# Kernel optimization log

Hardware: AMD Instinct MI355X
Metric: run time of the kernel (lower is better)

The kernel has to match this reference:

```python
import jax, jax.numpy as jnp
import numpy as np

NUM_USER = 200000
NUM_ITEM = 100000
DIM = 64
NUM_LAYER = 2  # hardcoded in LightGCN.__init__ (lgn_single(..., num_layer=2))
AVG_DEG = 16
N = NUM_USER + NUM_ITEM
E = N * AVG_DEG
BATCH = 16384


def setup_inputs() -> dict:
    key = jax.random.key(0)
    k = jax.random.split(key, 8)
    emb_user = jax.random.normal(k[0], (NUM_USER, DIM), jnp.float32) * 0.05
    emb_item = jax.random.normal(k[1], (NUM_ITEM, DIM), jnp.float32) * 0.05
    # COO sparse normalized adjacency: out[row] += vals * x[col]
    graph_row = jax.random.randint(k[2], (E,), 0, N, dtype=jnp.int32)
    graph_col = jax.random.randint(k[3], (E,), 0, N, dtype=jnp.int32)
    graph_vals = jax.random.uniform(k[4], (E,), jnp.float32) / AVG_DEG
    user_nodes = jax.random.randint(k[5], (BATCH,), 0, NUM_USER, dtype=jnp.int32)
    pos_item_nodes = jax.random.randint(k[6], (BATCH,), 0, NUM_ITEM, dtype=jnp.int32) + NUM_USER
    neg_item_nodes = jax.random.randint(k[7], (BATCH,), 0, NUM_ITEM, dtype=jnp.int32) + NUM_USER
    return {
        "emb_user": emb_user,
        "emb_item": emb_item,
        "graph_vals": graph_vals,
        "graph_row": graph_row,
        "graph_col": graph_col,
        "user_nodes": user_nodes,
        "pos_item_nodes": pos_item_nodes,
        "neg_item_nodes": neg_item_nodes,
    }


def _spmm(vals, row, col, x):
    # torch.sparse.mm(graph, x) with graph in COO form
    return jax.ops.segment_sum(vals[:, None] * x[col], row, num_segments=N)


def reference(emb_user, emb_item, graph_vals, graph_row, graph_col,
              user_nodes, pos_item_nodes, neg_item_nodes):
    # LGN_single.forward: concat, propagate, mean over layer stack
    all_emb = jnp.concatenate([emb_user, emb_item], axis=0)  # [N, D]
    acc = all_emb
    e = all_emb
    for _ in range(NUM_LAYER):
        e = _spmm(graph_vals, graph_row, graph_col, e)
        acc = acc + e
    light_out = acc / (NUM_LAYER + 1)  # mean of stacked embeddings
    # LightGCN.forward: gather + elementwise dot scores
    u = light_out[user_nodes]          # [B, D]
    p = light_out[pos_item_nodes]      # [B, D]
    n = light_out[neg_item_nodes]      # [B, D]
    pos_scores = jnp.sum(u * p, axis=1)
    neg_scores = jnp.sum(u * n, axis=1)
    return jnp.stack([pos_scores, neg_scores])  # [2, B]
```

## Files before the change

kernel.cpp:

```cpp
#include <hip/hip_runtime.h>

#define DIM 64
#define CHUNK 16384
#define MAXNB 512
#define BSHIFT 10
#define RPB 1024
#define PADMASK 7

union H8 { uint4 u; _Float16 h[8]; };
union H4 { uint2 u; _Float16 h[4]; };

__device__ __forceinline__ int blockScan256(int v, int* sh) {
    int t = threadIdx.x;
    sh[t] = v;
    __syncthreads();
    for (int off = 1; off < 256; off <<= 1) {
        int x = (t >= off) ? sh[t - off] : 0;
        __syncthreads();
        sh[t] += x;
        __syncthreads();
    }
    return sh[t];
}


__global__ void conv2_k(const float* __restrict__ u, const float* __restrict__ it,
                        int nu, int ntot, unsigned short* __restrict__ o) {
    int i = blockIdx.x * blockDim.x + threadIdx.x;
    int stride = gridDim.x * blockDim.x;
    int n8 = ntot >> 3;
    for (int t = i; t < n8; t += stride) {
        int e = t * 8;
        const float* src = (e < nu) ? (u + e) : (it + (e - nu));
        float4 x = *(const float4*)src;
        float4 y = *(const float4*)(src + 4);
        H8 v;
        v.h[0] = (_Float16)x.x; v.h[1] = (_Float16)x.y;
        v.h[2] = (_Float16)x.z; v.h[3] = (_Float16)x.w;
        v.h[4] = (_Float16)y.x; v.h[5] = (_Float16)y.y;
        v.h[6] = (_Float16)y.z; v.h[7] = (_Float16)y.w;
        ((uint4*)o)[t] = v.u;
    }
}


__global__ void p1a_hist(const int* __restrict__ row, int E, int NB,
                         int* __restrict__ counts) {
    __shared__ int h[MAXNB];
    for (int b = threadIdx.x; b < NB; b += 256) h[b] = 0;
    __syncthreads();
    int base = blockIdx.x * CHUNK;
    int end = min(base + CHUNK, E);
    int vend = base + ((end - base) & ~3);
    for (int i = base + threadIdx.x * 4; i < vend; i += 1024) {
        int4 r = *(const int4*)(row + i);
        atomicAdd(&h[r.x >> BSHIFT], 1);
        atomicAdd(&h[r.y >> BSHIFT], 1);
        atomicAdd(&h[r.z >> BSHIFT], 1);
        atomicAdd(&h[r.w >> BSHIFT], 1);
    }
    for (int i = vend + threadIdx.x; i < end; i += 256) atomicAdd(&h[row[i] >> BSHIFT], 1);
    __syncthreads();
    int blk = blockIdx.x;
    for (int b = threadIdx.x; b < NB; b += 256) counts[(size_t)blk * NB + b] = h[b];
}

__global__ void p1b_scan(int* __restrict__ counts, int NBLK, int NB,
                         int* __restrict__ bucketTotal) {
    int b = blockIdx.x, t = threadIdx.x;
    __shared__ int sh[256];
    int v[8];
    int run = 0;
#pragma unroll
    for (int i = 0; i < 8; i++) {
        int idx = t * 8 + i;
        int c = (idx < NBLK) ? counts[(size_t)idx * NB + b] : 0;
        v[i] = run;
        run += c;
    }
    int inc = blockScan256(run, sh);
    int excl = inc - run;
#pragma unroll
    for (int i = 0; i < 8; i++) {
        int idx = t * 8 + i;
        if (idx < NBLK) counts[(size_t)idx * NB + b] = v[i] + excl;
    }
    if (t == 255) bucketTotal[b] = sh[255];
}

__global__ void p_scan_tot(const int* __restrict__ bucketTotal, int NB,
                           int* __restrict__ bucketStart) {
    int t = threadIdx.x;
    __shared__ int sh[256];
    int v[8];
    int run = 0;
#pragma unroll
    for (int i = 0; i < 8; i++) {
        int idx = t * 8 + i;
        int c = (idx < NB) ? bucketTotal[idx] : 0;
        v[i] = run;
        run += c;
    }
    int inc = blockScan256(run, sh);
    int excl = inc - run;
#pragma unroll
    for (int i = 0; i < 8; i++) {
        int idx = t * 8 + i;
        if (idx < NB) bucketStart[idx] = v[i] + excl;
    }
    if (t == 255) bucketStart[NB] = sh[255];
}

__global__ void p1c_scatter(const int* __restrict__ row, const int* __restrict__ col,
                            const float* __restrict__ vals, int E, int NB,
                            const int* __restrict__ counts, const int* __restrict__ bucketStart,
                            int2* __restrict__ bdata) {
    __shared__ int cur[MAXNB];
    int blk = blockIdx.x;
    for (int b = threadIdx.x; b < NB; b += 256)
        cur[b] = bucketStart[b] + counts[(size_t)blk * NB + b];
    __syncthreads();
    int base = blk * CHUNK;
    int end = min(base + CHUNK, E);
    int vend = base + ((end - base) & ~3);
    for (int i = base + threadIdx.x * 4; i < vend; i += 1024) {
        int4 r = *(const int4*)(row + i);
        int4 c = *(const int4*)(col + i);
        float4 v = *(const float4*)(vals + i);
        int p0 = atomicAdd(&cur[r.x >> BSHIFT], 1);
        int p1 = atomicAdd(&cur[r.y >> BSHIFT], 1);
        int p2 = atomicAdd(&cur[r.z >> BSHIFT], 1);
        int p3 = atomicAdd(&cur[r.w >> BSHIFT], 1);
        bdata[p0] = make_int2(((r.x & (RPB - 1)) << 20) | c.x, __float_as_int(v.x));
        bdata[p1] = make_int2(((r.y & (RPB - 1)) << 20) | c.y, __float_as_int(v.y));
        bdata[p2] = make_int2(((r.z & (RPB - 1)) << 20) | c.z, __float_as_int(v.z));
        bdata[p3] = make_int2(((r.w & (RPB - 1)) << 20) | c.w, __float_as_int(v.w));
    }
    for (int i = vend + threadIdx.x; i < end; i += 256) {
        int r = row[i];
        int p = atomicAdd(&cur[r >> BSHIFT], 1);
        bdata[p] = make_int2(((r & (RPB - 1)) << 20) | col[i], __float_as_int(vals[i]));
    }
}

__global__ void p2_group(const int2* __restrict__ bdata, const int* __restrict__ bucketStart,
                         int NB, int N, int padSlop,
                         int* __restrict__ rowStart, int* __restrict__ rowLen,
                         int2* __restrict__ pairs) {
    __shared__ int hist[RPB];
    __shared__ int sh[256];
    __shared__ int cur[RPB];
    int b = blockIdx.x, t = threadIdx.x;
    int s0 = bucketStart[b], s1 = bucketStart[b + 1];
    int pbase = s0 + b * padSlop;
    for (int i = t; i < RPB; i += 256) hist[i] = 0;
    __syncthreads();
    for (int i = s0 + t; i < s1; i += 256)
        atomicAdd(&hist[(bdata[i].x >> 20) & (RPB - 1)], 1);
    __syncthreads();
    int v[4];
    int run = 0;
#pragma unroll
    for (int i = 0; i < 4; i++) {
        int h = hist[t * 4 + i];
        int hp = (h + PADMASK) & ~PADMASK;
        v[i] = run;
        run += hp;
    }
    int inc = blockScan256(run, sh);
    int excl = inc - run;
#pragma unroll
    for (int i = 0; i < 4; i++) {
        int r = (b << BSHIFT) + t * 4 + i;
        int st = excl + v[i];
        if (r < N) {
            int h = hist[t * 4 + i];
            rowStart[r] = pbase + st;
            rowLen[r] = (h + PADMASK) & ~PADMASK;
        }
        cur[t * 4 + i] = st;
    }
    __syncthreads();
    for (int i = s0 + t; i < s1; i += 256) {
        int2 e = bdata[i];
        int rl = (e.x >> 20) & (RPB - 1);
        int pos = atomicAdd(&cur[rl], 1);
        pairs[pbase + pos] = make_int2((e.x & 0xFFFFF) << 7, e.y);
    }
    __syncthreads();
#pragma unroll
    for (int i = 0; i < 4; i++) {
        int h = hist[t * 4 + i];
        int hp = (h + PADMASK) & ~PADMASK;
        int st = excl + v[i];
        for (int p = st + h; p < st + hp; p++)
            pairs[pbase + p] = make_int2(0, 0);
    }
}


__global__ void spmm1_k(const unsigned short* __restrict__ emb16,
                        const int* __restrict__ rowStart, const int* __restrict__ rowLen,
                        const int2* __restrict__ pairs,
                        int n_total, unsigned short* __restrict__ e1) {
    int wave = (blockIdx.x * blockDim.x + threadIdx.x) >> 6;
    int lane = threadIdx.x & 63;
    if (wave >= n_total) return;
    int eg = lane >> 3, dp = lane & 7;
    unsigned off0 = dp * 16u;
    const char* base = (const char*)emb16;
    int len = rowLen[wave];
    const int2* pp = pairs + rowStart[wave];
    float aA[8] = {0.f, 0.f, 0.f, 0.f, 0.f, 0.f, 0.f, 0.f};
    float aB[8] = {0.f, 0.f, 0.f, 0.f, 0.f, 0.f, 0.f, 0.f};
    int k = 0;
    for (; k + 16 <= len; k += 16) {
        int4 q = *(const int4*)(pp + k + 2 * eg);
        H8 g0, g1;
        g0.u = *(const uint4*)(base + ((unsigned)q.x + off0));
        g1.u = *(const uint4*)(base + ((unsigned)q.z + off0));
        float v0 = __int_as_float(q.y), v1 = __int_as_float(q.w);
#pragma unroll
        for (int i = 0; i < 8; i++) aA[i] += (float)g0.h[i] * v0;
#pragma unroll
        for (int i = 0; i < 8; i++) aB[i] += (float)g1.h[i] * v1;
    }
    if (k < len) {
        int2 p = pp[k + eg];
        H8 g0;
        g0.u = *(const uint4*)(base + ((unsigned)p.x + off0));
        float v0 = __int_as_float(p.y);
#pragma unroll
        for (int i = 0; i < 8; i++) aA[i] += (float)g0.h[i] * v0;
    }
    float s[8];
#pragma unroll
    for (int i = 0; i < 8; i++) s[i] = aA[i] + aB[i];
#pragma unroll
    for (int m = 8; m <= 32; m <<= 1) {
#pragma unroll
        for (int i = 0; i < 8; i++) s[i] += __shfl_xor(s[i], m);
    }
    if (eg == 0) {
        H8 o;
#pragma unroll
        for (int i = 0; i < 8; i++) o.h[i] = (_Float16)s[i];
        *(uint4*)(e1 + (size_t)wave * DIM + dp * 8) = o.u;
    }
}


__global__ void final_k(const float* __restrict__ emb_user, const float* __restrict__ emb_item,
                        int n_user, const unsigned short* __restrict__ e1,
                        const int* __restrict__ rowStart, const int* __restrict__ rowLen,
                        const int2* __restrict__ pairs,
                        const int* __restrict__ u_nodes, const int* __restrict__ p_nodes,
                        const int* __restrict__ n_nodes, int B, float* __restrict__ out) {
    int wave = (blockIdx.x * blockDim.x + threadIdx.x) >> 6;
    int lane = threadIdx.x & 63;
    if (wave >= B) return;
    int eg = lane >> 4, dp = lane & 15;
    unsigned off0 = dp * 8u;
    const char* base = (const char*)e1;
    int nid[3] = {u_nodes[wave], p_nodes[wave], n_nodes[wave]};
    float l[3][4];
#pragma unroll
    for (int j = 0; j < 3; j++) {
        int r = nid[j];
        const float* base0 = (r < n_user) ? (emb_user + (size_t)r * DIM)
                                          : (emb_item + (size_t)(r - n_user) * DIM);
        float4 l0 = *(const float4*)(base0 + dp * 4);
        H4 t1;
        t1.u = *(const uint2*)(e1 + (size_t)r * DIM + dp * 4);
        float acc[4];
        acc[0] = l0.x + (float)t1.h[0];
        acc[1] = l0.y + (float)t1.h[1];
        acc[2] = l0.z + (float)t1.h[2];
        acc[3] = l0.w + (float)t1.h[3];
        int len = rowLen[r];
        const int2* pp = pairs + rowStart[r];
        float a0[4] = {0.f, 0.f, 0.f, 0.f}, a1[4] = {0.f, 0.f, 0.f, 0.f};
        float a2[4] = {0.f, 0.f, 0.f, 0.f}, a3[4] = {0.f, 0.f, 0.f, 0.f};
        int k = 0;
        for (; k + 16 <= len; k += 16) {
            int4 q0 = *(const int4*)(pp + k + 2 * eg);
            int4 q1 = *(const int4*)(pp + k + 8 + 2 * eg);
            H4 g0, g1, g2, g3;
            g0.u = *(const uint2*)(base + ((unsigned)q0.x + off0));
            g1.u = *(const uint2*)(base + ((unsigned)q0.z + off0));
            g2.u = *(const uint2*)(base + ((unsigned)q1.x + off0));
            g3.u = *(const uint2*)(base + ((unsigned)q1.z + off0));
            float v0 = __int_as_float(q0.y), v1 = __int_as_float(q0.w);
            float v2 = __int_as_float(q1.y), v3 = __int_as_float(q1.w);
#pragma unroll
            for (int i = 0; i < 4; i++) {
                a0[i] += (float)g0.h[i] * v0;
                a1[i] += (float)g1.h[i] * v1;
                a2[i] += (float)g2.h[i] * v2;
                a3[i] += (float)g3.h[i] * v3;
            }
        }
        for (; k < len; k += 8) {
            int4 q0 = *(const int4*)(pp + k + 2 * eg);
            H4 g0, g1;
            g0.u = *(const uint2*)(base + ((unsigned)q0.x + off0));
            g1.u = *(const uint2*)(base + ((unsigned)q0.z + off0));
            float v0 = __int_as_float(q0.y), v1 = __int_as_float(q0.w);
#pragma unroll
            for (int i = 0; i < 4; i++) {
                a0[i] += (float)g0.h[i] * v0;
                a1[i] += (float)g1.h[i] * v1;
            }
        }
        float s[4];
#pragma unroll
        for (int i = 0; i < 4; i++) s[i] = (a0[i] + a1[i]) + (a2[i] + a3[i]);
#pragma unroll
        for (int i = 0; i < 4; i++) {
            s[i] += __shfl_xor(s[i], 16);
            s[i] += __shfl_xor(s[i], 32);
        }
#pragma unroll
        for (int i = 0; i < 4; i++) l[j][i] = (acc[i] + s[i]) * (1.0f / 3.0f);
    }
    float ps = l[0][0] * l[1][0] + l[0][1] * l[1][1] + l[0][2] * l[1][2] + l[0][3] * l[1][3];
    float ns = l[0][0] * l[2][0] + l[0][1] * l[2][1] + l[0][2] * l[2][2] + l[0][3] * l[2][3];
    ps += __shfl_xor(ps, 1); ns += __shfl_xor(ns, 1);
    ps += __shfl_xor(ps, 2); ns += __shfl_xor(ns, 2);
    ps += __shfl_xor(ps, 4); ns += __shfl_xor(ns, 4);
    ps += __shfl_xor(ps, 8); ns += __shfl_xor(ns, 8);
    if (lane == 0) {
        out[wave] = ps;
        out[B + wave] = ns;
    }
}

extern "C" void kernel_launch(void* const* d_in, const int* in_sizes, int n_in,
                              void* d_out, int out_size, void* d_ws, size_t ws_size,
                              hipStream_t stream) {
    const float* emb_user = (const float*)d_in[0];
    const float* emb_item = (const float*)d_in[1];
    const float* gvals    = (const float*)d_in[2];
    const int*   grow     = (const int*)d_in[3];
    const int*   gcol     = (const int*)d_in[4];
    const int*   unodes   = (const int*)d_in[5];
    const int*   pnodes   = (const int*)d_in[6];
    const int*   nnodes   = (const int*)d_in[7];
    float* out = (float*)d_out;

    int n_user = in_sizes[0] / DIM;
    int n_item = in_sizes[1] / DIM;
    int N = n_user + n_item;
    int E = in_sizes[2];
    int B = in_sizes[5];
    int NB = (N + RPB - 1) >> BSHIFT;
    int NBLK = (E + CHUNK - 1) / CHUNK;
    int padSlop = RPB * PADMASK;

    char* ws = (char*)d_ws;
    size_t off = 0;
    auto alloc = [&](size_t bytes) -> void* {
        void* p = ws + off;
        off = (off + bytes + 255) & ~(size_t)255;
        return p;
    };
    size_t embBytes = (size_t)N * DIM * 2;
    size_t countsBytes = (size_t)NBLK * NB * 4;
    size_t regionBBytes = (size_t)E * 8 > embBytes ? (size_t)E * 8 : embBytes;
    size_t regionABytes = countsBytes > embBytes ? countsBytes : embBytes;
    size_t pairsBytes = ((size_t)E + (size_t)NB * padSlop) * 8;

    int*  rowStart    = (int*)alloc((size_t)N * 4);
    int*  rowLen      = (int*)alloc((size_t)N * 4);
    int*  bucketTotal = (int*)alloc((size_t)MAXNB * 4);
    int*  bucketStart = (int*)alloc((size_t)(MAXNB + 1) * 4);
    int2* pairs       = (int2*)alloc(pairsBytes);
    char* regionB = (char*)alloc(regionBBytes);
    int2*           bdata = (int2*)regionB;
    unsigned short* emb16 = (unsigned short*)regionB;
    char* regionA = (char*)alloc(regionABytes);
    int*            counts = (int*)regionA;
    unsigned short* e1     = (unsigned short*)regionA;
    (void)n_in; (void)out_size; (void)ws_size;

    p1a_hist<<<NBLK, 256, 0, stream>>>(grow, E, NB, counts);
    p1b_scan<<<NB, 256, 0, stream>>>(counts, NBLK, NB, bucketTotal);
    p_scan_tot<<<1, 256, 0, stream>>>(bucketTotal, NB, bucketStart);
    p1c_scatter<<<NBLK, 256, 0, stream>>>(grow, gcol, gvals, E, NB, counts, bucketStart, bdata);
    p2_group<<<NB, 256, 0, stream>>>(bdata, bucketStart, NB, N, padSlop,
                                     rowStart, rowLen, pairs);

    conv2_k<<<2048, 256, 0, stream>>>(emb_user, emb_item, n_user * DIM, N * DIM, emb16);

    spmm1_k<<<(N + 3) / 4, 256, 0, stream>>>(emb16, rowStart, rowLen, pairs, N, e1);
    final_k<<<(B + 3) / 4, 256, 0, stream>>>(emb_user, emb_item, n_user, e1,
                                             rowStart, rowLen, pairs,
                                             unodes, pnodes, nnodes, B, out);
}
```

Before: 300.9 us.

## Stage bucket scatter in LDS and overlap fp16 conversion with histogram

The scatter kernel now sorts each chunk's edges by bucket in shared memory first. It then writes each bucket's run contiguously to global memory, replacing random per-edge global writes with coalesced ones. The per-block local offsets come from differencing the scanned counts. The fp16 embedding conversion is folded into extra blocks of the histogram kernel when the workspace allows separate buffers, removing a serial launch. CHUNK is halved so the 64KB staging buffer fits in LDS, which doubles the number of blocks and the size of the counts matrix.

```diff
diff --git a/kernel.cpp b/kernel.cpp
--- a/kernel.cpp
+++ b/kernel.cpp
@@ -1,11 +1,12 @@
 #include <hip/hip_runtime.h>
 
 #define DIM 64
-#define CHUNK 16384
+#define CHUNK 8192
 #define MAXNB 512
 #define BSHIFT 10
 #define RPB 1024
 #define PADMASK 7
+#define CONVB 768
 
 union H8 { uint4 u; _Float16 h[8]; };
 union H4 { uint2 u; _Float16 h[4]; };
@@ -23,13 +24,12 @@
     return sh[t];
 }
 
-
-__global__ void conv2_k(const float* __restrict__ u, const float* __restrict__ it,
-                        int nu, int ntot, unsigned short* __restrict__ o) {
-    int i = blockIdx.x * blockDim.x + threadIdx.x;
-    int stride = gridDim.x * blockDim.x;
+__device__ __forceinline__ void convBody(const float* __restrict__ u,
+                                         const float* __restrict__ it,
+                                         int nu, int ntot, unsigned short* __restrict__ o,
+                                         int start, int stride) {
     int n8 = ntot >> 3;
-    for (int t = i; t < n8; t += stride) {
+    for (int t = start; t < n8; t += stride) {
         int e = t * 8;
         const float* src = (e < nu) ? (u + e) : (it + (e - nu));
         float4 x = *(const float4*)src;
@@ -44,25 +44,38 @@
 }
 
 
-__global__ void p1a_hist(const int* __restrict__ row, int E, int NB,
-                         int* __restrict__ counts) {
+__global__ void p1a_conv(const int* __restrict__ row, int E, int NB,
+                         int* __restrict__ counts,
+                         const float* __restrict__ u, const float* __restrict__ it,
+                         int nu, int ntot, unsigned short* __restrict__ o, int NBLK) {
     __shared__ int h[MAXNB];
-    for (int b = threadIdx.x; b < NB; b += 256) h[b] = 0;
-    __syncthreads();
-    int base = blockIdx.x * CHUNK;
-    int end = min(base + CHUNK, E);
-    int vend = base + ((end - base) & ~3);
-    for (int i = base + threadIdx.x * 4; i < vend; i += 1024) {
-        int4 r = *(const int4*)(row + i);
-        atomicAdd(&h[r.x >> BSHIFT], 1);
-        atomicAdd(&h[r.y >> BSHIFT], 1);
-        atomicAdd(&h[r.z >> BSHIFT], 1);
-        atomicAdd(&h[r.w >> BSHIFT], 1);
-    }
-    for (int i = vend + threadIdx.x; i < end; i += 256) atomicAdd(&h[row[i] >> BSHIFT], 1);
-    __syncthreads();
     int blk = blockIdx.x;
-    for (int b = threadIdx.x; b < NB; b += 256) counts[(size_t)blk * NB + b] = h[b];
+    if (blk < NBLK) {
+        for (int b = threadIdx.x; b < NB; b += 256) h[b] = 0;
+        __syncthreads();
+        int base = blk * CHUNK;
+        int end = min(base + CHUNK, E);
+        int vend = base + ((end - base) & ~3);
+        for (int i = base + threadIdx.x * 4; i < vend; i += 1024) {
+            int4 r = *(const int4*)(row + i);
+            atomicAdd(&h[r.x >> BSHIFT], 1);
+            atomicAdd(&h[r.y >> BSHIFT], 1);
+            atomicAdd(&h[r.z >> BSHIFT], 1);
+            atomicAdd(&h[r.w >> BSHIFT], 1);
+        }
+        for (int i = vend + threadIdx.x; i < end; i += 256) atomicAdd(&h[row[i] >> BSHIFT], 1);
+        __syncthreads();
+        for (int b = threadIdx.x; b < NB; b += 256) counts[(size_t)blk * NB + b] = h[b];
+    } else {
+        int nConv = gridDim.x - NBLK;
+        convBody(u, it, nu, ntot, o, (blk - NBLK) * 256 + threadIdx.x, nConv * 256);
+    }
+}
+
+__global__ void conv2_k(const float* __restrict__ u, const float* __restrict__ it,
+                        int nu, int ntot, unsigned short* __restrict__ o) {
+    convBody(u, it, nu, ntot, o, blockIdx.x * blockDim.x + threadIdx.x,
+             gridDim.x * blockDim.x);
 }
 
 __global__ void p1b_scan(int* __restrict__ counts, int NBLK, int NB,
@@ -112,34 +125,66 @@
 }
 
 __global__ void p1c_scatter(const int* __restrict__ row, const int* __restrict__ col,
-                            const float* __restrict__ vals, int E, int NB,
-                            const int* __restrict__ counts, const int* __restrict__ bucketStart,
-                            int2* __restrict__ bdata) {
+                            const float* __restrict__ vals, int E, int NB, int NBLK,
+                            const int* __restrict__ counts, const int* __restrict__ bucketTotal,
+                            const int* __restrict__ bucketStart, int2* __restrict__ bdata) {
+    __shared__ int2 stage[CHUNK];
     __shared__ int cur[MAXNB];
-    int blk = blockIdx.x;
-    for (int b = threadIdx.x; b < NB; b += 256)
-        cur[b] = bucketStart[b] + counts[(size_t)blk * NB + b];
-    __syncthreads();
+    __shared__ int rawcnt[MAXNB];
+    __shared__ int sh[256];
+    int blk = blockIdx.x, t = threadIdx.x;
     int base = blk * CHUNK;
     int end = min(base + CHUNK, E);
+    int v[2];
+    int run = 0;
+#pragma unroll
+    for (int i = 0; i < 2; i++) {
+        int b = t * 2 + i;
+        int c = 0;
+        if (b < NB) {
+            int s0 = counts[(size_t)blk * NB + b];
+            int s1 = (blk + 1 < NBLK) ? counts[(size_t)(blk + 1) * NB + b] : bucketTotal[b];
+            c = s1 - s0;
+            rawcnt[b] = c;
+        }
+        v[i] = run;
+        run += c;
+    }
+    int inc = blockScan256(run, sh);
+    int excl = inc - run;
+#pragma unroll
+    for (int i = 0; i < 2; i++) {
+        int b = t * 2 + i;
+        if (b < NB) cur[b] = excl + v[i];
+    }
+    __syncthreads();
     int vend = base + ((end - base) & ~3);
-    for (int i = base + threadIdx.x * 4; i < vend; i += 1024) {
+    for (int i = base + t * 4; i < vend; i += 1024) {
         int4 r = *(const int4*)(row + i);
         int4 c = *(const int4*)(col + i);
-        float4 v = *(const float4*)(vals + i);
+        float4 w = *(const float4*)(vals + i);
         int p0 = atomicAdd(&cur[r.x >> BSHIFT], 1);
         int p1 = atomicAdd(&cur[r.y >> BSHIFT], 1);
         int p2 = atomicAdd(&cur[r.z >> BSHIFT], 1);
         int p3 = atomicAdd(&cur[r.w >> BSHIFT], 1);
-        bdata[p0] = make_int2(((r.x & (RPB - 1)) << 20) | c.x, __float_as_int(v.x));
-        bdata[p1] = make_int2(((r.y & (RPB - 1)) << 20) | c.y, __float_as_int(v.y));
-        bdata[p2] = make_int2(((r.z & (RPB - 1)) << 20) | c.z, __float_as_int(v.z));
-        bdata[p3] = make_int2(((r.w & (RPB - 1)) << 20) | c.w, __float_as_int(v.w));
-    }
-    for (int i = vend + threadIdx.x; i < end; i += 256) {
+        stage[p0] = make_int2(((r.x & (RPB - 1)) << 20) | c.x, __float_as_int(w.x));
+        stage[p1] = make_int2(((r.y & (RPB - 1)) << 20) | c.y, __float_as_int(w.y));
+        stage[p2] = make_int2(((r.z & (RPB - 1)) << 20) | c.z, __float_as_int(w.z));
+        stage[p3] = make_int2(((r.w & (RPB - 1)) << 20) | c.w, __float_as_int(w.w));
+    }
+    for (int i = vend + t; i < end; i += 256) {
         int r = row[i];
         int p = atomicAdd(&cur[r >> BSHIFT], 1);
-        bdata[p] = make_int2(((r & (RPB - 1)) << 20) | col[i], __float_as_int(vals[i]));
+        stage[p] = make_int2(((r & (RPB - 1)) << 20) | col[i], __float_as_int(vals[i]));
+    }
+    __syncthreads();
+    int wv = t >> 6, lane = t & 63;
+    for (int b = wv; b < NB; b += 4) {
+        int cnt = rawcnt[b];
+        int lo = cur[b] - cnt;
+        int gb = bucketStart[b] + counts[(size_t)blk * NB + b];
+        for (int i = lane; i < cnt; i += 64)
+            bdata[gb + i] = stage[lo + i];
     }
 }
 
@@ -357,6 +402,17 @@
     int NBLK = (E + CHUNK - 1) / CHUNK;
     int padSlop = RPB * PADMASK;
 
+    auto align256 = [](size_t x) { return (x + 255) & ~(size_t)255; };
+    size_t embBytes = (size_t)N * DIM * 2;
+    size_t countsBytes = (size_t)NBLK * NB * 4;
+    size_t bdataBytes = (size_t)E * 8;
+    size_t regionABytes = countsBytes > embBytes ? countsBytes : embBytes;
+    size_t pairsBytes = ((size_t)E + (size_t)NB * padSlop) * 8;
+    size_t fixedBytes = align256((size_t)N * 4) * 2 + align256((size_t)MAXNB * 4) +
+                        align256((size_t)(MAXNB + 1) * 4) + align256(pairsBytes) +
+                        align256(regionABytes);
+    bool sepEmb = fixedBytes + align256(bdataBytes) + align256(embBytes) <= ws_size;
+
     char* ws = (char*)d_ws;
     size_t off = 0;
     auto alloc = [&](size_t bytes) -> void* {
@@ -364,33 +420,38 @@
         off = (off + bytes + 255) & ~(size_t)255;
         return p;
     };
-    size_t embBytes = (size_t)N * DIM * 2;
-    size_t countsBytes = (size_t)NBLK * NB * 4;
-    size_t regionBBytes = (size_t)E * 8 > embBytes ? (size_t)E * 8 : embBytes;
-    size_t regionABytes = countsBytes > embBytes ? countsBytes : embBytes;
-    size_t pairsBytes = ((size_t)E + (size_t)NB * padSlop) * 8;
-
     int*  rowStart    = (int*)alloc((size_t)N * 4);
     int*  rowLen      = (int*)alloc((size_t)N * 4);
     int*  bucketTotal = (int*)alloc((size_t)MAXNB * 4);
     int*  bucketStart = (int*)alloc((size_t)(MAXNB + 1) * 4);
     int2* pairs       = (int2*)alloc(pairsBytes);
-    char* regionB = (char*)alloc(regionBBytes);
-    int2*           bdata = (int2*)regionB;
-    unsigned short* emb16 = (unsigned short*)regionB;
+    int2* bdata;
+    unsigned short* emb16;
+    if (sepEmb) {
+        bdata = (int2*)alloc(bdataBytes);
+        emb16 = (unsigned short*)alloc(embBytes);
+    } else {
+        char* regionB = (char*)alloc(bdataBytes > embBytes ? bdataBytes : embBytes);
+        bdata = (int2*)regionB;
+        emb16 = (unsigned short*)regionB;
+    }
     char* regionA = (char*)alloc(regionABytes);
     int*            counts = (int*)regionA;
     unsigned short* e1     = (unsigned short*)regionA;
-    (void)n_in; (void)out_size; (void)ws_size;
-
-    p1a_hist<<<NBLK, 256, 0, stream>>>(grow, E, NB, counts);
+    (void)n_in; (void)out_size;
+
+    int nConv = sepEmb ? CONVB : 0;
+    p1a_conv<<<NBLK + nConv, 256, 0, stream>>>(grow, E, NB, counts,
+                                               emb_user, emb_item, n_user * DIM, N * DIM,
+                                               emb16, NBLK);
     p1b_scan<<<NB, 256, 0, stream>>>(counts, NBLK, NB, bucketTotal);
     p_scan_tot<<<1, 256, 0, stream>>>(bucketTotal, NB, bucketStart);
-    p1c_scatter<<<NBLK, 256, 0, stream>>>(grow, gcol, gvals, E, NB, counts, bucketStart, bdata);
+    p1c_scatter<<<NBLK, 256, 0, stream>>>(grow, gcol, gvals, E, NB, NBLK,
+                                          counts, bucketTotal, bucketStart, bdata);
     p2_group<<<NB, 256, 0, stream>>>(bdata, bucketStart, NB, N, padSlop,
                                      rowStart, rowLen, pairs);
-
-    conv2_k<<<2048, 256, 0, stream>>>(emb_user, emb_item, n_user * DIM, N * DIM, emb16);
+    if (!sepEmb)
+        conv2_k<<<2048, 256, 0, stream>>>(emb_user, emb_item, n_user * DIM, N * DIM, emb16);
 
     spmm1_k<<<(N + 3) / 4, 256, 0, stream>>>(emb16, rowStart, rowLen, pairs, N, e1);
     final_k<<<(B + 3) / 4, 256, 0, stream>>>(emb_user, emb_item, n_user, e1,
```

New measurement: 293.0 us (median of 2 runs). -2.6%, faster.
